# Kernel tuning notes

Hardware: AMD Instinct MI355X
Metric: run time of the kernel (lower is better)

## Reference

```python
import jax, jax.numpy as jnp
import numpy as np

SIGMA = 1.0
KSIZE = 5
WEAK = 75.0
STRONG = 255.0
LOW_T = 0.00392
HIGH_T = 0.15

# scipy.signal.gaussian(M, std): unnormalized gaussian window
_n = np.arange(KSIZE, dtype=np.float32) - (KSIZE - 1) / 2.0
_g = np.exp(-0.5 * (_n / SIGMA) ** 2).astype(np.float32)
GAUSS_H = jnp.asarray(_g.reshape(1, 1, 1, KSIZE))  # horizontal 1xK
GAUSS_V = jnp.asarray(_g.reshape(1, 1, KSIZE, 1))  # vertical Kx1

_sobel = np.array([[1, 0, -1], [2, 0, -2], [1, 0, -1]], dtype=np.float32)
SOBEL_H = jnp.asarray(_sobel.reshape(1, 1, 3, 3))
SOBEL_V = jnp.asarray(_sobel.T.reshape(1, 1, 3, 3))

_f0 = np.array([[0, 0, 0], [0, 1, -1], [0, 0, 0]], np.float32)
_f45 = np.array([[0, 0, 0], [0, 1, 0], [0, 0, -1]], np.float32)
_f90 = np.array([[0, 0, 0], [0, 1, 0], [0, -1, 0]], np.float32)
_f135 = np.array([[0, 0, 0], [0, 1, 0], [-1, 0, 0]], np.float32)
_f180 = np.array([[0, 0, 0], [-1, 1, 0], [0, 0, 0]], np.float32)
_f225 = np.array([[-1, 0, 0], [0, 1, 0], [0, 0, 0]], np.float32)
_f270 = np.array([[0, -1, 0], [0, 1, 0], [0, 0, 0]], np.float32)
_f315 = np.array([[0, 0, -1], [0, 1, 0], [0, 0, 0]], np.float32)
DIR_FILT = jnp.asarray(np.stack([_f0, _f45, _f90, _f135, _f180, _f225, _f270, _f315]).reshape(8, 1, 3, 3))

NBR_FILT = jnp.asarray(np.array([[1, 1, 1], [1, 0, 1], [1, 1, 1]], np.float32).reshape(1, 1, 3, 3))


def _conv(x, w, pad):
    # cross-correlation, matching torch F.conv2d
    return jax.lax.conv_general_dilated(
        x, w, window_strides=(1, 1), padding=[(pad[0], pad[0]), (pad[1], pad[1])],
        dimension_numbers=('NCHW', 'OIHW', 'NCHW'))


def setup_inputs() -> dict:
    key = jax.random.key(0)
    img = jax.random.uniform(key, (16, 1, 1024, 1024), dtype=jnp.float32)
    return {"img": img}


def reference(img):
    B = img.shape[0]
    # --- gaussian noise removal (separable) ---
    sm = _conv(img, GAUSS_H, (0, KSIZE // 2))
    sm = _conv(sm, GAUSS_V, (KSIZE // 2, 0))
    # --- sobel gradients ---
    Ix = _conv(sm, SOBEL_H, (1, 1))
    Iy = _conv(sm, SOBEL_V, (1, 1))
    mag = jnp.sqrt(Ix ** 2 + Iy ** 2)
    mag = mag / mag.reshape(B, -1).max(axis=1).reshape(B, 1, 1, 1)
    direction = jnp.arctan2(Iy, Ix) * (180.0 / 3.1415926) + 180.0
    direction = jnp.round(direction / 45.0) * 45.0
    # --- non-max suppression via directional differences + gather ---
    all_filtered = _conv(mag, DIR_FILT, (1, 1))  # [B,8,H,W]
    idx_pos = (direction / 45.0).astype(jnp.int32) % 8  # [B,1,H,W]
    idx_neg = (idx_pos + 4) % 8
    cs_pos = jnp.take_along_axis(all_filtered, idx_pos, axis=1)
    cs_neg = jnp.take_along_axis(all_filtered, idx_neg, axis=1)
    is_max = jnp.minimum(cs_pos, cs_neg) > 0.0
    thin = jnp.where(is_max, mag, 0.0)
    # --- double threshold ---
    hi = thin.max() * HIGH_T  # global max, as in source
    strong = thin >= hi
    weak = (thin < hi) & (thin >= LOW_T)
    inter = jnp.where(strong, STRONG, jnp.where(weak, WEAK, 0.0))
    # --- hysteresis: iterate until no weak pixel gains a strong neighbor ---
    def cond(state):
        return state[1]

    def body(state):
        x, _ = state
        weak_m = x == WEAK
        sn = _conv((x == STRONG).astype(jnp.float32), NBR_FILT, (1, 1))
        new_strong = weak_m & (sn > 0.0)
        x = jnp.where(new_strong, STRONG, x)
        return x, new_strong.any()

    final, _ = jax.lax.while_loop(cond, body, (inter, jnp.asarray(True)))
    final = jnp.where(final == STRONG, final, 0.0)
    return final
```

## Files before the change

### kernel.cpp

```cpp
#include <hip/hip_runtime.h>
#include <math.h>

#define BB 16
#define H 1024
#define W 1024
#define HW (H*W)
#define NTOT (BB*HW)

typedef unsigned long long u64;

__device__ __constant__ float GW[5] = {
    0.13533528323661270f, 0.60653065971263342f, 1.0f,
    0.60653065971263342f, 0.13533528323661270f};

#define CSCALE ((float)(180.0 / 3.1415926))

#define TW 128
#define TH 8
__global__ __launch_bounds__(256, 8) void k_smooth_sobel(const float* __restrict__ img,
                                                         float* __restrict__ mag,
                                                         unsigned char* __restrict__ bucket,
                                                         float* __restrict__ partial) {
#pragma clang fp contract(off)
    __shared__ float sA[14 * 136 + 16];
    __shared__ float sB[14 * 132];
    __shared__ float red[256];

    const int tid = threadIdx.x;
    const int x0 = blockIdx.x * TW;
    const int y0 = blockIdx.y * TH;
    const int b = blockIdx.z;
    const size_t base = (size_t)b * HW;

    for (int idx = tid; idx < 14 * 34; idx += 256) {
        int r = idx / 34, v = idx - r * 34;
        int gy = y0 - 3 + r;
        int gxv = x0 - 4 + v * 4;
        float4 val = make_float4(0.f, 0.f, 0.f, 0.f);
        if (gy >= 0 && gy < H && gxv >= 0 && gxv <= W - 4)
            val = *(const float4*)&img[base + (size_t)gy * W + gxv];
        *(float4*)&sA[r * 136 + v * 4] = val;
    }
    __syncthreads();

    for (int idx = tid; idx < 14 * 33; idx += 256) {
        int r = idx / 33, g = idx - r * 33;
        const float* p = &sA[r * 136 + g * 4];
        float4 A0 = *(const float4*)p;
        float4 A1 = *(const float4*)(p + 4);
        float4 A2 = *(const float4*)(p + 8);
        float a_[12] = {A0.x, A0.y, A0.z, A0.w, A1.x, A1.y, A1.z, A1.w,
                        A2.x, A2.y, A2.z, A2.w};
        float o[4];
#pragma unroll
        for (int j = 0; j < 4; ++j) {
            float s = 0.0f;
#pragma unroll
            for (int k = 0; k < 5; ++k) s = s + GW[k] * a_[j + 1 + k];
            o[j] = s;
        }
        *(float4*)&sB[r * 132 + g * 4] = make_float4(o[0], o[1], o[2], o[3]);
    }
    __syncthreads();

    for (int idx = tid; idx < 10 * 33; idx += 256) {
        int rr = idx / 33, g = idx - rr * 33;
        float bb[20];
#pragma unroll
        for (int k = 0; k < 5; ++k) {
            float4 t = *(const float4*)&sB[(rr + k) * 132 + g * 4];
            bb[k * 4 + 0] = t.x; bb[k * 4 + 1] = t.y;
            bb[k * 4 + 2] = t.z; bb[k * 4 + 3] = t.w;
        }
        int gy = y0 - 1 + rr;
        bool rowok = (gy >= 0 && gy < H);
        float o[4];
#pragma unroll
        for (int j = 0; j < 4; ++j) {
            float s = 0.0f;
#pragma unroll
            for (int k = 0; k < 5; ++k) s = s + GW[k] * bb[k * 4 + j];
            int gx = x0 - 1 + g * 4 + j;
            o[j] = (rowok && gx >= 0 && gx < W) ? s : 0.0f;
        }
        *(float4*)&sA[rr * 136 + g * 4] = make_float4(o[0], o[1], o[2], o[3]);
    }
    __syncthreads();

    const int r = tid >> 5;
    const int cg = (tid & 31) * 4;
    const int y = y0 + r;
    const float* P0 = &sA[r * 136 + cg];
    const float* P1 = P0 + 136;
    const float* P2 = P1 + 136;
    float4 q0 = *(const float4*)P0; float2 e0 = *(const float2*)(P0 + 4);
    float4 q1 = *(const float4*)P1; float2 e1 = *(const float2*)(P1 + 4);
    float4 q2 = *(const float4*)P2; float2 e2 = *(const float2*)(P2 + 4);
    float r0[6] = {q0.x, q0.y, q0.z, q0.w, e0.x, e0.y};
    float r1[6] = {q1.x, q1.y, q1.z, q1.w, e1.x, e1.y};
    float r2[6] = {q2.x, q2.y, q2.z, q2.w, e2.x, e2.y};

    float tmax = 0.0f;
    float mg[4];
    unsigned int bk = 0;
#pragma unroll
    for (int j = 0; j < 4; ++j) {
        float a00 = r0[j], a01 = r0[j + 1], a02 = r0[j + 2];
        float a10 = r1[j],                  a12 = r1[j + 2];
        float a20 = r2[j], a21 = r2[j + 1], a22 = r2[j + 2];

        float Ix = a00;
        Ix = Ix - a02;
        Ix = Ix + 2.0f * a10;
        Ix = Ix - 2.0f * a12;
        Ix = Ix + a20;
        Ix = Ix - a22;

        float Iy = a00;
        Iy = Iy + 2.0f * a01;
        Iy = Iy + a02;
        Iy = Iy - a20;
        Iy = Iy - 2.0f * a21;
        Iy = Iy - a22;

        float t1 = Ix * Ix;
        float t2 = Iy * Iy;
        float m = sqrtf(t1 + t2);
        mg[j] = m;
        tmax = fmaxf(tmax, m);

        float ax = fabsf(Ix), ay = fabsf(Iy);
        float mn = fminf(ax, ay), mx = fmaxf(ax, ay);
        float cr = mn * 0.92387953f - mx * 0.38268343f;
        int bidx;
        if (fabsf(cr) < mx * 3e-5f) {
            float fa2 = (float)atan2((double)Iy, (double)Ix);
            float d2 = fa2 * CSCALE;
            d2 = d2 + 180.0f;
            float t2d = d2 / 45.0f;
            float rr2 = rintf(t2d);
            bidx = ((int)rr2) & 7;
        } else if (ay <= ax * 0.41421356f) {
            bidx = signbit(Ix) ? 0 : 4;
        } else if (ay >= ax * 2.41421356f) {
            bidx = (Iy >= 0.0f) ? 6 : 2;
        } else {
            bidx = (Iy >= 0.0f) ? ((Ix >= 0.0f) ? 5 : 7)
                                : ((Ix >= 0.0f) ? 3 : 1);
        }
        bk |= ((unsigned int)bidx) << (8 * j);
    }
    *(float4*)&mag[base + (size_t)y * W + x0 + cg] = make_float4(mg[0], mg[1], mg[2], mg[3]);
    *(unsigned int*)&bucket[base + (size_t)y * W + x0 + cg] = bk;

    red[tid] = tmax;
    __syncthreads();
    for (int s = 128; s > 0; s >>= 1) {
        if (tid < s) red[tid] = fmaxf(red[tid], red[tid + s]);
        __syncthreads();
    }
    if (tid == 0) {
        int pb = (blockIdx.z * 128 + blockIdx.y) * 8 + blockIdx.x;
        partial[pb] = red[0];
    }
}

__global__ __launch_bounds__(256) void k_redmax_img(const float* __restrict__ partial,
                                                    float* __restrict__ magmax) {
    __shared__ float red[256];
    const float* p = partial + blockIdx.x * 1024;
    float m = 0.0f;
    for (int k = threadIdx.x; k < 1024; k += 256) m = fmaxf(m, p[k]);
    red[threadIdx.x] = m;
    __syncthreads();
    for (int s = 128; s > 0; s >>= 1) {
        if (threadIdx.x < s) red[threadIdx.x] = fmaxf(red[threadIdx.x], red[threadIdx.x + s]);
        __syncthreads();
    }
    if (threadIdx.x == 0) magmax[blockIdx.x] = red[0];
}

__global__ __launch_bounds__(256, 8) void k_nms_b2(const float* __restrict__ mag,
                                                   const unsigned char* __restrict__ bucket,
                                                   const float* __restrict__ magmax,
                                                   u64* __restrict__ Mb,
                                                   float* __restrict__ partial) {
#pragma clang fp contract(off)
    __shared__ float sN[34 * 136];
    __shared__ float red[256];

    const int tid = threadIdx.x;
    const int x0 = blockIdx.x * 128;
    const int y0 = blockIdx.y * 32;
    const int b = blockIdx.z;
    const size_t base = (size_t)b * HW;
    const float M = magmax[b];

    for (int idx = tid; idx < 34 * 34; idx += 256) {
        int r = idx / 34, v = idx - r * 34;
        int gy = y0 - 1 + r;
        int gxv = x0 - 4 + v * 4;
        float4 val = make_float4(0.f, 0.f, 0.f, 0.f);
        if (gy >= 0 && gy < H && gxv >= 0 && gxv <= W - 4)
            val = *(const float4*)&mag[base + (size_t)gy * W + gxv];
        *(float4*)&sN[r * 136 + v * 4] = val;
    }
    __syncthreads();

    const int L = tid & 63, wv = tid >> 6;
    const int h = wv & 1, wr = wv >> 1;
    const int c = h * 64 + L;
    const int txw = (x0 >> 6) + h;
    float amax = 0.0f;

#pragma unroll 4
    for (int i = 0; i < 16; ++i) {
        const int r = i * 2 + wr;
        const int y = y0 + r;
        int bkt = bucket[base + (size_t)y * W + x0 + c];
        int t1 = (bkt + 1) & 7;
        int dy = ((bkt >= 1 && bkt <= 3) ? 1 : 0) - ((bkt >= 5) ? 1 : 0);
        int dx = ((t1 <= 2) ? 1 : 0) - ((t1 >= 4 && t1 <= 6) ? 1 : 0);

        const int o = (r + 1) * 136 + c + 4;
        const int od = dy * 136 + dx;
        float a  = sN[o];
        float bp = sN[o + od];
        float bn = sN[o - od];

        bool g1 = a > bp, g2 = a > bn;
        bool f1 = a >= bp * 1.0000005f;
        bool f2 = a >= bn * 1.0000005f;
        bool im = g1 && g2;
        bool bad = (g1 && !f1) || (g2 && !f2);
        if (__any(bad)) {
            if (bad) {
                float qa = a / M;
                bool r1 = g1, r2 = g2;
                if (g1 && !f1) r1 = qa > (bp / M);
                if (g2 && !f2) r2 = qa > (bn / M);
                im = r1 && r2;
            }
        }
        if (im) amax = fmaxf(amax, a);
        u64 word = __ballot(im);
        if (L == 0) Mb[((b << 8) | ((y >> 6) << 4) | txw) * 64 + (y & 63)] = word;
    }

    red[tid] = amax;
    __syncthreads();
    for (int s = 128; s > 0; s >>= 1) {
        if (tid < s) red[tid] = fmaxf(red[tid], red[tid + s]);
        __syncthreads();
    }
    if (tid == 0)
        partial[(blockIdx.z * 32 + blockIdx.y) * 8 + blockIdx.x] = red[0] / M;
}

__global__ __launch_bounds__(1024) void k_finalize_thr(const float* __restrict__ partial,
                                                       float* __restrict__ hdr,
                                                       float* __restrict__ thr) {
    __shared__ float red[1024];
    float m = 0.0f;
    for (int k = threadIdx.x; k < 4096; k += 1024) m = fmaxf(m, partial[k]);
    red[threadIdx.x] = m;
    __syncthreads();
    for (int s = 512; s > 0; s >>= 1) {
        if (threadIdx.x < s) red[threadIdx.x] = fmaxf(red[threadIdx.x], red[threadIdx.x + s]);
        __syncthreads();
    }
    if (threadIdx.x == 0) hdr[16] = red[0];
    if (threadIdx.x < 32) {
        float tm = red[0];
        int t = threadIdx.x;
        float M = hdr[t >> 1];
        float T = (t & 1) ? (tm * 0.15f) : 0.00392f;
        if (0.0f / M >= T) { thr[t] = 0.0f; return; }
        unsigned int lo = 0u, hi = 0x7f800000u;
        while (hi - lo > 1u) {
            unsigned int mid = lo + ((hi - lo) >> 1);
            if (__uint_as_float(mid) / M >= T) hi = mid; else lo = mid;
        }
        thr[t] = __uint_as_float(hi);
    }
}

__global__ __launch_bounds__(256, 8) void k_thresh_w(const float* __restrict__ mag,
                                                     const u64* __restrict__ Mb,
                                                     const float* __restrict__ hdr,
                                                     const float* __restrict__ thr,
                                                     u64* __restrict__ Sb,
                                                     u64* __restrict__ Wb) {
    const int tid = threadIdx.x;
    const int L = tid & 63, wv = tid >> 6;
    const int h = wv & 1, wr = wv >> 1;
    const int x0 = blockIdx.x * 128;
    const int y0 = blockIdx.y * 32;
    const int b = blockIdx.z;
    const size_t base = (size_t)b * HW;
    const float Alo = thr[b * 2], Ahi = thr[b * 2 + 1];
    const bool snm = (hdr[16] * 0.15f <= 0.0f);
    const int txw = (x0 >> 6) + h;

#pragma unroll 4
    for (int i = 0; i < 16; ++i) {
        const int r = i * 2 + wr;
        const int y = y0 + r;
        const int widx = ((b << 8) | ((y >> 6) << 4) | txw) * 64 + (y & 63);
        float a = mag[base + (size_t)y * W + x0 + h * 64 + L];
        u64 mw = Mb[widx];
        bool im = (mw >> L) & 1ull;
        bool strong = snm || (im && (a >= Ahi));
        bool weak = (!strong) && im && (a >= Alo);
        u64 sw = __ballot(strong);
        u64 ww = __ballot(weak);
        if (L == 0) { Sb[widx] = sw; Wb[widx] = ww; }
    }
}

template <bool LAST>
__global__ __launch_bounds__(256) void k_hyster_bits(const u64* __restrict__ Wb,
                                                     u64* __restrict__ Sb,
                                                     float* __restrict__ out) {
    const int lane = threadIdx.x & 63;
    const int t = blockIdx.x * 4 + (threadIdx.x >> 6);
    const int ty = (t >> 4) & 15;
    const int tx = t & 15;
    const int idx = t * 64 + lane;

    u64 S = Sb[idx];
    const u64 Wk = Wb[idx];

    u64 hstat = 0;
    if (tx > 0)  hstat |= (Sb[(t - 1) * 64 + lane] >> 63) & 1ull;
    if (tx < 15) hstat |= (Sb[(t + 1) * 64 + lane] & 1ull) << 63;

    u64 halo = 0;
    if (lane == 0 && ty > 0) {
        const int ta = t - 16;
        u64 tc = Sb[ta * 64 + 63];
        u64 hh = (tc << 1) | tc | (tc >> 1);
        if (tx > 0)  hh |= (Sb[(ta - 1) * 64 + 63] >> 63) & 1ull;
        if (tx < 15) hh |= (Sb[(ta + 1) * 64 + 63] & 1ull) << 63;
        halo = hh;
    }
    if (lane == 63 && ty < 15) {
        const int tb = t + 16;
        u64 tc = Sb[tb * 64 + 0];
        u64 hh = (tc << 1) | tc | (tc >> 1);
        if (tx > 0)  hh |= (Sb[(tb - 1) * 64 + 0] >> 63) & 1ull;
        if (tx < 15) hh |= (Sb[(tb + 1) * 64 + 0] & 1ull) << 63;
        halo = hh;
    }

    for (int it = 0; it < 160; ++it) {
        u64 hh = (S << 1) | S | (S >> 1) | hstat;
        u64 up = __shfl_up(hh, 1, 64);
        if (lane == 0) up = halo;
        u64 dn = __shfl_down(hh, 1, 64);
        if (lane == 63) dn = halo;
        u64 dil = hh | up | dn;
        u64 nS = S | (Wk & dil);
        bool ch = (nS != S);
        S = nS;
        if (!__any(ch)) break;
    }

    if (!LAST) {
        Sb[idx] = S;
    } else {
        const int bimg = t >> 8;
        float* op = out + (size_t)bimg * HW + (size_t)(ty * 64) * W + tx * 64 + lane;
#pragma unroll 4
        for (int rr = 0; rr < 64; ++rr) {
            u64 wrow = __shfl(S, rr, 64);
            op[(size_t)rr * W] = ((wrow >> lane) & 1ull) ? 255.0f : 0.0f;
        }
    }
}

extern "C" void kernel_launch(void* const* d_in, const int* in_sizes, int n_in,
                              void* d_out, int out_size, void* d_ws, size_t ws_size,
                              hipStream_t stream) {
    (void)in_sizes; (void)n_in; (void)out_size; (void)ws_size;
    const float* img = (const float*)d_in[0];
    float* out = (float*)d_out;

    float* hdr = (float*)d_ws;
    float* thr = hdr + 64;
    float* partialA = hdr + 128;
    float* partialB = partialA + 16384;
    float* A = partialB + 4096;
    unsigned char* C = (unsigned char*)(A + (size_t)NTOT);
    u64* Sb = (u64*)(C + (size_t)NTOT);
    u64* Wb = Sb + NTOT / 64;
    u64* Mb = Wb + NTOT / 64;

    dim3 blk(256);
    k_smooth_sobel<<<dim3(8, 128, BB), blk, 0, stream>>>(img, A, C, partialA);
    k_redmax_img<<<dim3(BB), blk, 0, stream>>>(partialA, hdr);
    k_nms_b2<<<dim3(8, 32, BB), blk, 0, stream>>>(A, C, hdr, Mb, partialB);
    k_finalize_thr<<<dim3(1), dim3(1024), 0, stream>>>(partialB, hdr, thr);
    k_thresh_w<<<dim3(8, 32, BB), blk, 0, stream>>>(A, Mb, hdr, thr, Sb, Wb);
    for (int p = 0; p < 5; ++p)
        k_hyster_bits<false><<<dim3(NTOT / (64 * 64) / 4), blk, 0, stream>>>(Wb, Sb, out);
    k_hyster_bits<true><<<dim3(NTOT / (64 * 64) / 4), blk, 0, stream>>>(Wb, Sb, out);
}
```

Measured before the change: 257.4 us.

## Fuse smoothing, Sobel and non-max suppression into one kernel with deferred fixup list

Merges the smooth/Sobel kernel and the NMS kernel into a single kernel. It recomputes magnitude over a one-pixel halo in shared memory, so the full magnitude and direction-bucket arrays no longer make a round trip through global memory. Ambiguous comparisons that need the per-image max are appended to a global list via atomics and resolved by a small fixup kernel, which also feeds a corrected thin-max into threshold finalization. The cost is extra halo recomputation, more shared memory per block, a single-block fixup pass, a memset, and a list capped at a fixed capacity.

```diff
diff --git a/kernel.cpp b/kernel.cpp
--- a/kernel.cpp
+++ b/kernel.cpp
@@ -6,6 +6,7 @@
 #define W 1024
 #define HW (H*W)
 #define NTOT (BB*HW)
+#define LISTCAP 65536
 
 typedef unsigned long long u64;
 
@@ -15,26 +16,28 @@
 
 #define CSCALE ((float)(180.0 / 3.1415926))
 
-#define TW 128
-#define TH 8
-__global__ __launch_bounds__(256, 8) void k_smooth_sobel(const float* __restrict__ img,
-                                                         float* __restrict__ mag,
-                                                         unsigned char* __restrict__ bucket,
-                                                         float* __restrict__ partial) {
+__global__ __launch_bounds__(256, 8) void k_mega(const float* __restrict__ img,
+                                                 float* __restrict__ mag,
+                                                 u64* __restrict__ Mb,
+                                                 float* __restrict__ partialA,
+                                                 float* __restrict__ partialT,
+                                                 unsigned int* __restrict__ list,
+                                                 unsigned int* __restrict__ cnt) {
 #pragma clang fp contract(off)
-    __shared__ float sA[14 * 136 + 16];
-    __shared__ float sB[14 * 132];
+    __shared__ float sA[16 * 136 + 16];
+    __shared__ float sB[16 * 132];
     __shared__ float red[256];
+    __shared__ unsigned int nib32[256];
 
     const int tid = threadIdx.x;
-    const int x0 = blockIdx.x * TW;
-    const int y0 = blockIdx.y * TH;
+    const int x0 = blockIdx.x * 128;
+    const int y0 = blockIdx.y * 8;
     const int b = blockIdx.z;
     const size_t base = (size_t)b * HW;
 
-    for (int idx = tid; idx < 14 * 34; idx += 256) {
+    for (int idx = tid; idx < 16 * 34; idx += 256) {
         int r = idx / 34, v = idx - r * 34;
-        int gy = y0 - 3 + r;
+        int gy = y0 - 4 + r;
         int gxv = x0 - 4 + v * 4;
         float4 val = make_float4(0.f, 0.f, 0.f, 0.f);
         if (gy >= 0 && gy < H && gxv >= 0 && gxv <= W - 4)
@@ -43,27 +46,25 @@
     }
     __syncthreads();
 
-    for (int idx = tid; idx < 14 * 33; idx += 256) {
+    for (int idx = tid; idx < 16 * 33; idx += 256) {
         int r = idx / 33, g = idx - r * 33;
         const float* p = &sA[r * 136 + g * 4];
         float4 A0 = *(const float4*)p;
         float4 A1 = *(const float4*)(p + 4);
-        float4 A2 = *(const float4*)(p + 8);
-        float a_[12] = {A0.x, A0.y, A0.z, A0.w, A1.x, A1.y, A1.z, A1.w,
-                        A2.x, A2.y, A2.z, A2.w};
+        float a_[8] = {A0.x, A0.y, A0.z, A0.w, A1.x, A1.y, A1.z, A1.w};
         float o[4];
 #pragma unroll
         for (int j = 0; j < 4; ++j) {
             float s = 0.0f;
 #pragma unroll
-            for (int k = 0; k < 5; ++k) s = s + GW[k] * a_[j + 1 + k];
+            for (int k = 0; k < 5; ++k) s = s + GW[k] * a_[j + k];
             o[j] = s;
         }
         *(float4*)&sB[r * 132 + g * 4] = make_float4(o[0], o[1], o[2], o[3]);
     }
     __syncthreads();
 
-    for (int idx = tid; idx < 10 * 33; idx += 256) {
+    for (int idx = tid; idx < 12 * 33; idx += 256) {
         int rr = idx / 33, g = idx - rr * 33;
         float bb[20];
 #pragma unroll
@@ -72,7 +73,7 @@
             bb[k * 4 + 0] = t.x; bb[k * 4 + 1] = t.y;
             bb[k * 4 + 2] = t.z; bb[k * 4 + 3] = t.w;
         }
-        int gy = y0 - 1 + rr;
+        int gy = y0 - 2 + rr;
         bool rowok = (gy >= 0 && gy < H);
         float o[4];
 #pragma unroll
@@ -80,95 +81,194 @@
             float s = 0.0f;
 #pragma unroll
             for (int k = 0; k < 5; ++k) s = s + GW[k] * bb[k * 4 + j];
+            int gx = x0 - 2 + g * 4 + j;
+            o[j] = (rowok && gx >= 0 && gx < W) ? s : 0.0f;
+        }
+        *(float4*)&sA[rr * 136 + g * 4] = make_float4(o[0], o[1], o[2], o[3]);
+    }
+    __syncthreads();
+
+    float tmax = 0.0f;
+    for (int idx = tid; idx < 330; idx += 256) {
+        int r = idx / 33, g = idx - r * 33;
+        int gy = y0 - 1 + r;
+        bool rowok = (gy >= 0 && gy < H);
+        const float* P0 = &sA[r * 136 + g * 4];
+        const float* P1 = P0 + 136;
+        const float* P2 = P1 + 136;
+        float4 q0 = *(const float4*)P0; float2 e0 = *(const float2*)(P0 + 4);
+        float4 q1 = *(const float4*)P1; float2 e1 = *(const float2*)(P1 + 4);
+        float4 q2 = *(const float4*)P2; float2 e2 = *(const float2*)(P2 + 4);
+        float r0[6] = {q0.x, q0.y, q0.z, q0.w, e0.x, e0.y};
+        float r1[6] = {q1.x, q1.y, q1.z, q1.w, e1.x, e1.y};
+        float r2[6] = {q2.x, q2.y, q2.z, q2.w, e2.x, e2.y};
+        int nj = (g < 32) ? 4 : 2;
+        float mg[4] = {0.f, 0.f, 0.f, 0.f};
+#pragma unroll
+        for (int j = 0; j < 4; ++j) {
+            if (j >= nj) continue;
+            float a00 = r0[j], a01 = r0[j + 1], a02 = r0[j + 2];
+            float a10 = r1[j],                  a12 = r1[j + 2];
+            float a20 = r2[j], a21 = r2[j + 1], a22 = r2[j + 2];
+            float Ix = a00;
+            Ix = Ix - a02;
+            Ix = Ix + 2.0f * a10;
+            Ix = Ix - 2.0f * a12;
+            Ix = Ix + a20;
+            Ix = Ix - a22;
+            float Iy = a00;
+            Iy = Iy + 2.0f * a01;
+            Iy = Iy + a02;
+            Iy = Iy - a20;
+            Iy = Iy - 2.0f * a21;
+            Iy = Iy - a22;
+            float t1 = Ix * Ix;
+            float t2 = Iy * Iy;
+            float m = sqrtf(t1 + t2);
             int gx = x0 - 1 + g * 4 + j;
-            o[j] = (rowok && gx >= 0 && gx < W) ? s : 0.0f;
-        }
-        *(float4*)&sA[rr * 136 + g * 4] = make_float4(o[0], o[1], o[2], o[3]);
-    }
-    __syncthreads();
-
-    const int r = tid >> 5;
-    const int cg = (tid & 31) * 4;
-    const int y = y0 + r;
-    const float* P0 = &sA[r * 136 + cg];
-    const float* P1 = P0 + 136;
-    const float* P2 = P1 + 136;
-    float4 q0 = *(const float4*)P0; float2 e0 = *(const float2*)(P0 + 4);
-    float4 q1 = *(const float4*)P1; float2 e1 = *(const float2*)(P1 + 4);
-    float4 q2 = *(const float4*)P2; float2 e2 = *(const float2*)(P2 + 4);
-    float r0[6] = {q0.x, q0.y, q0.z, q0.w, e0.x, e0.y};
-    float r1[6] = {q1.x, q1.y, q1.z, q1.w, e1.x, e1.y};
-    float r2[6] = {q2.x, q2.y, q2.z, q2.w, e2.x, e2.y};
-
-    float tmax = 0.0f;
-    float mg[4];
-    unsigned int bk = 0;
-#pragma unroll
-    for (int j = 0; j < 4; ++j) {
-        float a00 = r0[j], a01 = r0[j + 1], a02 = r0[j + 2];
-        float a10 = r1[j],                  a12 = r1[j + 2];
-        float a20 = r2[j], a21 = r2[j + 1], a22 = r2[j + 2];
-
-        float Ix = a00;
-        Ix = Ix - a02;
-        Ix = Ix + 2.0f * a10;
-        Ix = Ix - 2.0f * a12;
-        Ix = Ix + a20;
-        Ix = Ix - a22;
-
-        float Iy = a00;
-        Iy = Iy + 2.0f * a01;
-        Iy = Iy + a02;
-        Iy = Iy - a20;
-        Iy = Iy - 2.0f * a21;
-        Iy = Iy - a22;
-
-        float t1 = Ix * Ix;
-        float t2 = Iy * Iy;
-        float m = sqrtf(t1 + t2);
-        mg[j] = m;
-        tmax = fmaxf(tmax, m);
-
-        float ax = fabsf(Ix), ay = fabsf(Iy);
-        float mn = fminf(ax, ay), mx = fmaxf(ax, ay);
-        float cr = mn * 0.92387953f - mx * 0.38268343f;
-        int bidx;
-        if (fabsf(cr) < mx * 3e-5f) {
-            float fa2 = (float)atan2((double)Iy, (double)Ix);
-            float d2 = fa2 * CSCALE;
-            d2 = d2 + 180.0f;
-            float t2d = d2 / 45.0f;
-            float rr2 = rintf(t2d);
-            bidx = ((int)rr2) & 7;
-        } else if (ay <= ax * 0.41421356f) {
-            bidx = signbit(Ix) ? 0 : 4;
-        } else if (ay >= ax * 2.41421356f) {
-            bidx = (Iy >= 0.0f) ? 6 : 2;
+            bool ok = rowok && (gx >= 0) && (gx < W);
+            m = ok ? m : 0.0f;
+            mg[j] = m;
+            tmax = fmaxf(tmax, m);
+        }
+        if (g < 32) {
+            *(float4*)&sB[r * 132 + g * 4] = make_float4(mg[0], mg[1], mg[2], mg[3]);
         } else {
-            bidx = (Iy >= 0.0f) ? ((Ix >= 0.0f) ? 5 : 7)
-                                : ((Ix >= 0.0f) ? 3 : 1);
-        }
-        bk |= ((unsigned int)bidx) << (8 * j);
-    }
-    *(float4*)&mag[base + (size_t)y * W + x0 + cg] = make_float4(mg[0], mg[1], mg[2], mg[3]);
-    *(unsigned int*)&bucket[base + (size_t)y * W + x0 + cg] = bk;
-
-    red[tid] = tmax;
-    __syncthreads();
+            sB[r * 132 + 128] = mg[0];
+            sB[r * 132 + 129] = mg[1];
+        }
+    }
+    __syncthreads();
+
+    {
+        const int r = tid >> 5;
+        const int cg = (tid & 31) * 4;
+        const int y = y0 + r;
+        const float* P0 = &sA[(r + 1) * 136 + cg];
+        const float* P1 = P0 + 136;
+        const float* P2 = P1 + 136;
+        float4 q0a = *(const float4*)P0, q0b = *(const float4*)(P0 + 4);
+        float4 q1a = *(const float4*)P1, q1b = *(const float4*)(P1 + 4);
+        float4 q2a = *(const float4*)P2, q2b = *(const float4*)(P2 + 4);
+        float R0[8] = {q0a.x, q0a.y, q0a.z, q0a.w, q0b.x, q0b.y, q0b.z, q0b.w};
+        float R1[8] = {q1a.x, q1a.y, q1a.z, q1a.w, q1b.x, q1b.y, q1b.z, q1b.w};
+        float R2[8] = {q2a.x, q2a.y, q2a.z, q2a.w, q2b.x, q2b.y, q2b.z, q2b.w};
+
+        float am[4];
+        unsigned int nib = 0;
+        float amax = 0.0f;
+#pragma unroll
+        for (int j = 0; j < 4; ++j) {
+            float a00 = R0[j + 1], a01 = R0[j + 2], a02 = R0[j + 3];
+            float a10 = R1[j + 1],                   a12 = R1[j + 3];
+            float a20 = R2[j + 1], a21 = R2[j + 2], a22 = R2[j + 3];
+            float Ix = a00;
+            Ix = Ix - a02;
+            Ix = Ix + 2.0f * a10;
+            Ix = Ix - 2.0f * a12;
+            Ix = Ix + a20;
+            Ix = Ix - a22;
+            float Iy = a00;
+            Iy = Iy + 2.0f * a01;
+            Iy = Iy + a02;
+            Iy = Iy - a20;
+            Iy = Iy - 2.0f * a21;
+            Iy = Iy - a22;
+
+            float ax = fabsf(Ix), ay = fabsf(Iy);
+            float mn = fminf(ax, ay), mx = fmaxf(ax, ay);
+            float crb = mn * 0.92387953f - mx * 0.38268343f;
+            int dy, dx;
+            if (fabsf(crb) < mx * 3e-5f) {
+                float fa2 = (float)atan2((double)Iy, (double)Ix);
+                float d2 = fa2 * CSCALE;
+                d2 = d2 + 180.0f;
+                float t2d = d2 / 45.0f;
+                float rr2 = rintf(t2d);
+                int bidx = ((int)rr2) & 7;
+                int t1 = (bidx + 1) & 7;
+                dy = ((bidx >= 1 && bidx <= 3) ? 1 : 0) - ((bidx >= 5) ? 1 : 0);
+                dx = ((t1 <= 2) ? 1 : 0) - ((t1 >= 4 && t1 <= 6) ? 1 : 0);
+            } else if (ay <= ax * 0.41421356f) {
+                dy = 0; dx = 1;
+            } else if (ay >= ax * 2.41421356f) {
+                dy = 1; dx = 0;
+            } else {
+                bool sameq = (Iy >= 0.0f) == (Ix >= 0.0f);
+                dy = 1; dx = sameq ? 1 : -1;
+            }
+
+            const int mo = (r + 1) * 132 + cg + 1 + j;
+            const int od = dy * 132 + dx;
+            float a  = sB[mo];
+            float bp = sB[mo + od];
+            float bn = sB[mo - od];
+            am[j] = a;
+
+            bool g1 = a > bp, g2 = a > bn;
+            bool f1 = a >= bp * 1.0000005f;
+            bool f2 = a >= bn * 1.0000005f;
+            bool im = g1 && g2;
+            bool bad = (g1 && !f1) || (g2 && !f2);
+            if (im && bad) {
+                unsigned int pos = atomicAdd(cnt, 1u);
+                if (pos < LISTCAP) {
+                    int xcol = cg + j;
+                    int widx = ((b << 8) | ((y >> 6) << 4) | ((x0 >> 6) + (xcol >> 6))) * 64 + (y & 63);
+                    unsigned int meta = ((unsigned int)widx << 10) |
+                                        ((unsigned int)(xcol & 63) << 4) | (unsigned int)b;
+                    unsigned int* rec = list + (size_t)pos * 4;
+                    rec[0] = __float_as_uint(a);
+                    rec[1] = __float_as_uint(bp);
+                    rec[2] = __float_as_uint(bn);
+                    rec[3] = meta;
+                }
+            }
+            if (im) {
+                nib |= 1u << j;
+                if (!bad) amax = fmaxf(amax, a);
+            }
+        }
+        *(float4*)&mag[base + (size_t)y * W + x0 + cg] = make_float4(am[0], am[1], am[2], am[3]);
+        nib32[tid] = nib;
+        red[tid] = amax;
+    }
+    __syncthreads();
+
+    if (tid < 16) {
+        int rw = tid >> 1, h = tid & 1;
+        u64 w = 0;
+#pragma unroll
+        for (int j = 0; j < 16; ++j)
+            w |= (u64)nib32[rw * 32 + h * 16 + j] << (4 * j);
+        int yy = y0 + rw;
+        int widx = ((b << 8) | ((yy >> 6) << 4) | ((x0 >> 6) + h)) * 64 + (yy & 63);
+        Mb[widx] = w;
+    }
+
     for (int s = 128; s > 0; s >>= 1) {
         if (tid < s) red[tid] = fmaxf(red[tid], red[tid + s]);
         __syncthreads();
     }
-    if (tid == 0) {
-        int pb = (blockIdx.z * 128 + blockIdx.y) * 8 + blockIdx.x;
-        partial[pb] = red[0];
-    }
-}
-
-__global__ __launch_bounds__(256) void k_redmax_img(const float* __restrict__ partial,
-                                                    float* __restrict__ magmax) {
+    const int pb = (blockIdx.z * 128 + blockIdx.y) * 8 + blockIdx.x;
+    if (tid == 0) partialT[pb] = red[0];
+    __syncthreads();
+
+    red[tid] = tmax;
+    __syncthreads();
+    for (int s = 128; s > 0; s >>= 1) {
+        if (tid < s) red[tid] = fmaxf(red[tid], red[tid + s]);
+        __syncthreads();
+    }
+    if (tid == 0) partialA[pb] = red[0];
+}
+
+__global__ __launch_bounds__(256) void k_redmax2(const float* __restrict__ pA,
+                                                 const float* __restrict__ pT,
+                                                 float* __restrict__ hdr,
+                                                 float* __restrict__ thinraw) {
     __shared__ float red[256];
-    const float* p = partial + blockIdx.x * 1024;
+    const float* p = pA + blockIdx.x * 1024;
     float m = 0.0f;
     for (int k = threadIdx.x; k < 1024; k += 256) m = fmaxf(m, p[k]);
     red[threadIdx.x] = m;
@@ -177,104 +277,74 @@
         if (threadIdx.x < s) red[threadIdx.x] = fmaxf(red[threadIdx.x], red[threadIdx.x + s]);
         __syncthreads();
     }
-    if (threadIdx.x == 0) magmax[blockIdx.x] = red[0];
-}
-
-__global__ __launch_bounds__(256, 8) void k_nms_b2(const float* __restrict__ mag,
-                                                   const unsigned char* __restrict__ bucket,
-                                                   const float* __restrict__ magmax,
-                                                   u64* __restrict__ Mb,
-                                                   float* __restrict__ partial) {
+    if (threadIdx.x == 0) hdr[blockIdx.x] = red[0];
+    __syncthreads();
+    const float* q = pT + blockIdx.x * 1024;
+    m = 0.0f;
+    for (int k = threadIdx.x; k < 1024; k += 256) m = fmaxf(m, q[k]);
+    red[threadIdx.x] = m;
+    __syncthreads();
+    for (int s = 128; s > 0; s >>= 1) {
+        if (threadIdx.x < s) red[threadIdx.x] = fmaxf(red[threadIdx.x], red[threadIdx.x + s]);
+        __syncthreads();
+    }
+    if (threadIdx.x == 0) thinraw[blockIdx.x] = red[0];
+}
+
+__global__ void k_fixup(const float* __restrict__ hdr,
+                        const unsigned int* __restrict__ list,
+                        const unsigned int* __restrict__ cnt,
+                        u64* __restrict__ Mb,
+                        unsigned int* __restrict__ extraU) {
 #pragma clang fp contract(off)
-    __shared__ float sN[34 * 136];
-    __shared__ float red[256];
-
-    const int tid = threadIdx.x;
-    const int x0 = blockIdx.x * 128;
-    const int y0 = blockIdx.y * 32;
-    const int b = blockIdx.z;
-    const size_t base = (size_t)b * HW;
-    const float M = magmax[b];
-
-    for (int idx = tid; idx < 34 * 34; idx += 256) {
-        int r = idx / 34, v = idx - r * 34;
-        int gy = y0 - 1 + r;
-        int gxv = x0 - 4 + v * 4;
-        float4 val = make_float4(0.f, 0.f, 0.f, 0.f);
-        if (gy >= 0 && gy < H && gxv >= 0 && gxv <= W - 4)
-            val = *(const float4*)&mag[base + (size_t)gy * W + gxv];
-        *(float4*)&sN[r * 136 + v * 4] = val;
-    }
-    __syncthreads();
-
-    const int L = tid & 63, wv = tid >> 6;
-    const int h = wv & 1, wr = wv >> 1;
-    const int c = h * 64 + L;
-    const int txw = (x0 >> 6) + h;
-    float amax = 0.0f;
-
-#pragma unroll 4
-    for (int i = 0; i < 16; ++i) {
-        const int r = i * 2 + wr;
-        const int y = y0 + r;
-        int bkt = bucket[base + (size_t)y * W + x0 + c];
-        int t1 = (bkt + 1) & 7;
-        int dy = ((bkt >= 1 && bkt <= 3) ? 1 : 0) - ((bkt >= 5) ? 1 : 0);
-        int dx = ((t1 <= 2) ? 1 : 0) - ((t1 >= 4 && t1 <= 6) ? 1 : 0);
-
-        const int o = (r + 1) * 136 + c + 4;
-        const int od = dy * 136 + dx;
-        float a  = sN[o];
-        float bp = sN[o + od];
-        float bn = sN[o - od];
-
+    unsigned int n = *cnt;
+    if (n > LISTCAP) n = LISTCAP;
+    for (unsigned int i = threadIdx.x; i < n; i += 256) {
+        const unsigned int* rec = list + (size_t)i * 4;
+        float a = __uint_as_float(rec[0]);
+        float bp = __uint_as_float(rec[1]);
+        float bn = __uint_as_float(rec[2]);
+        unsigned int meta = rec[3];
+        int b = meta & 15;
+        int bit = (meta >> 4) & 63;
+        int widx = meta >> 10;
+        float M = hdr[b];
         bool g1 = a > bp, g2 = a > bn;
         bool f1 = a >= bp * 1.0000005f;
         bool f2 = a >= bn * 1.0000005f;
-        bool im = g1 && g2;
-        bool bad = (g1 && !f1) || (g2 && !f2);
-        if (__any(bad)) {
-            if (bad) {
-                float qa = a / M;
-                bool r1 = g1, r2 = g2;
-                if (g1 && !f1) r1 = qa > (bp / M);
-                if (g2 && !f2) r2 = qa > (bn / M);
-                im = r1 && r2;
-            }
-        }
-        if (im) amax = fmaxf(amax, a);
-        u64 word = __ballot(im);
-        if (L == 0) Mb[((b << 8) | ((y >> 6) << 4) | txw) * 64 + (y & 63)] = word;
-    }
-
-    red[tid] = amax;
-    __syncthreads();
-    for (int s = 128; s > 0; s >>= 1) {
-        if (tid < s) red[tid] = fmaxf(red[tid], red[tid + s]);
-        __syncthreads();
-    }
-    if (tid == 0)
-        partial[(blockIdx.z * 32 + blockIdx.y) * 8 + blockIdx.x] = red[0] / M;
-}
-
-__global__ __launch_bounds__(1024) void k_finalize_thr(const float* __restrict__ partial,
-                                                       float* __restrict__ hdr,
-                                                       float* __restrict__ thr) {
-    __shared__ float red[1024];
-    float m = 0.0f;
-    for (int k = threadIdx.x; k < 4096; k += 1024) m = fmaxf(m, partial[k]);
-    red[threadIdx.x] = m;
-    __syncthreads();
-    for (int s = 512; s > 0; s >>= 1) {
-        if (threadIdx.x < s) red[threadIdx.x] = fmaxf(red[threadIdx.x], red[threadIdx.x + s]);
-        __syncthreads();
-    }
-    if (threadIdx.x == 0) hdr[16] = red[0];
-    if (threadIdx.x < 32) {
-        float tm = red[0];
-        int t = threadIdx.x;
+        bool r1 = g1, r2 = g2;
+        float qa = a / M;
+        if (g1 && !f1) r1 = qa > (bp / M);
+        if (g2 && !f2) r2 = qa > (bn / M);
+        if (r1 && r2) atomicMax(&extraU[b], __float_as_uint(a));
+        else atomicAnd(&Mb[widx], ~(1ull << bit));
+    }
+}
+
+__global__ void k_finalize2(const float* __restrict__ thinraw,
+                            const unsigned int* __restrict__ extraU,
+                            float* __restrict__ hdr,
+                            float* __restrict__ thr) {
+#pragma clang fp contract(off)
+    __shared__ float timg[16];
+    __shared__ float tms;
+    int t = threadIdx.x;
+    if (t < 16) {
+        float M = hdr[t];
+        float raw = fmaxf(thinraw[t], __uint_as_float(extraU[t]));
+        timg[t] = raw / M;
+    }
+    __syncthreads();
+    if (t == 0) {
+        float m = 0.0f;
+        for (int i = 0; i < 16; ++i) m = fmaxf(m, timg[i]);
+        hdr[16] = m;
+        tms = m;
+    }
+    __syncthreads();
+    if (t < 32) {
         float M = hdr[t >> 1];
-        float T = (t & 1) ? (tm * 0.15f) : 0.00392f;
+        float T = (t & 1) ? (tms * 0.15f) : 0.00392f;
         if (0.0f / M >= T) { thr[t] = 0.0f; return; }
         unsigned int lo = 0u, hi = 0x7f800000u;
         while (hi - lo > 1u) {
@@ -387,20 +457,25 @@
     float* out = (float*)d_out;
 
     float* hdr = (float*)d_ws;
+    unsigned int* extraU = (unsigned int*)(hdr + 32);
+    unsigned int* cnt = (unsigned int*)(hdr + 48);
     float* thr = hdr + 64;
+    float* thinraw = hdr + 96;
     float* partialA = hdr + 128;
-    float* partialB = partialA + 16384;
-    float* A = partialB + 4096;
-    unsigned char* C = (unsigned char*)(A + (size_t)NTOT);
-    u64* Sb = (u64*)(C + (size_t)NTOT);
+    float* partialT = partialA + 16384;
+    unsigned int* list = (unsigned int*)(partialT + 16384);
+    float* A = (float*)(list + (size_t)LISTCAP * 4);
+    u64* Sb = (u64*)(A + (size_t)NTOT);
     u64* Wb = Sb + NTOT / 64;
     u64* Mb = Wb + NTOT / 64;
 
+    hipMemsetAsync(d_ws, 0, 256, stream);
+
     dim3 blk(256);
-    k_smooth_sobel<<<dim3(8, 128, BB), blk, 0, stream>>>(img, A, C, partialA);
-    k_redmax_img<<<dim3(BB), blk, 0, stream>>>(partialA, hdr);
-    k_nms_b2<<<dim3(8, 32, BB), blk, 0, stream>>>(A, C, hdr, Mb, partialB);
-    k_finalize_thr<<<dim3(1), dim3(1024), 0, stream>>>(partialB, hdr, thr);
+    k_mega<<<dim3(8, 128, BB), blk, 0, stream>>>(img, A, Mb, partialA, partialT, list, cnt);
+    k_redmax2<<<dim3(BB), blk, 0, stream>>>(partialA, partialT, hdr, thinraw);
+    k_fixup<<<dim3(1), blk, 0, stream>>>(hdr, list, cnt, Mb, extraU);
+    k_finalize2<<<dim3(1), dim3(64), 0, stream>>>(thinraw, extraU, hdr, thr);
     k_thresh_w<<<dim3(8, 32, BB), blk, 0, stream>>>(A, Mb, hdr, thr, Sb, Wb);
     for (int p = 0; p < 5; ++p)
         k_hyster_bits<false><<<dim3(NTOT / (64 * 64) / 4), blk, 0, stream>>>(Wb, Sb, out);
```

New measurement: 259.7 us. Within noise of the previous version (+0.9%).
